# Kernel tuning notes

Measured on AMD Instinct MI355X. Metric: run time of the kernel, lower is better.

## Reference

```python
import jax, jax.numpy as jnp
import numpy as np

B, N, C, H = 8, 4096, 768, 8
EPS = 1e-12  # F.normalize eps


def setup_inputs() -> dict:
    key = jax.random.key(0)
    ks = jax.random.split(key, 4)
    x = jax.random.normal(ks[0], (B, N, C), dtype=jnp.float32)
    w_qkv = jax.random.normal(ks[1], (3 * C, C), dtype=jnp.float32) * 0.02
    temperature = jnp.ones((H, 1, 1), dtype=jnp.float32)
    w_proj = jax.random.normal(ks[2], (C, C), dtype=jnp.float32) * 0.02
    b_proj = jnp.zeros((C,), dtype=jnp.float32)
    return {"x": x, "w_qkv": w_qkv, "temperature": temperature,
            "w_proj": w_proj, "b_proj": b_proj}


def _l2norm(t):
    # F.normalize(t, dim=-1): t / max(||t||_2, eps)
    n = jnp.sqrt(jnp.sum(t * t, axis=-1, keepdims=True))
    return t / jnp.maximum(n, EPS)


def reference(x, w_qkv, temperature, w_proj, b_proj):
    b, n, c = x.shape
    h = H
    hd = c // h
    # qkv projection: (B,N,3C) -> (3,B,H,hd,N)
    qkv = (x @ w_qkv.T).reshape(b, n, 3, h, hd)
    qkv = jnp.transpose(qkv, (2, 0, 3, 4, 1))
    q, k, v = qkv[0], qkv[1], qkv[2]          # each (B,H,hd,N)
    qn = _l2norm(q)                            # normalize over N (token) dim
    kn = _l2norm(k)
    # small per-head covariance attention: (B,H,hd,hd)
    attn = jnp.einsum('bhdn,bhen->bhde', qn, kn) * temperature
    attn = jax.nn.softmax(attn, axis=-1)
    out = jnp.einsum('bhde,bhen->bhdn', attn, v)  # (B,H,hd,N)
    out = jnp.transpose(out, (0, 3, 1, 2)).reshape(b, n, c)
    return out @ w_proj.T + b_proj
```

## Files before the change

### kernel.cpp

```cpp
#include <hip/hip_runtime.h>
#include <cstdint>
#include <cstddef>

#define B_ 8
#define N_ 4096
#define C_ 768
#define H_ 8
#define HD_ 96
#define EPSN 1e-12f
#define NS_ 4

typedef short s16x8 __attribute__((ext_vector_type(8)));
typedef short s16x4 __attribute__((ext_vector_type(4)));
typedef float f32x4 __attribute__((ext_vector_type(4)));

static __device__ __forceinline__ short f2bf(float f) {
  unsigned u = __float_as_uint(f);
  unsigned r = (u + 0x7fff + ((u >> 16) & 1)) >> 16;
  return (short)r;
}
static __device__ __forceinline__ float bf2f(unsigned short s) {
  return __uint_as_float(((unsigned)s) << 16);
}
static __device__ __forceinline__ s16x8 pack8(const float4 a, const float4 b) {
  s16x8 r;
  r[0] = f2bf(a.x); r[1] = f2bf(a.y); r[2] = f2bf(a.z); r[3] = f2bf(a.w);
  r[4] = f2bf(b.x); r[5] = f2bf(b.y); r[6] = f2bf(b.z); r[7] = f2bf(b.w);
  return r;
}

#define TSW(ch, t) ((t) ^ ((((ch) >> 2) & 7) << 3))

static __device__ __forceinline__ int swz(int s) {
  return s ^ (((s >> 7) & 3) << 3);
}

static __device__ __forceinline__ void gld16(const short* g, short* l) {
  __builtin_amdgcn_global_load_lds(
      (const __attribute__((address_space(1))) void*)g,
      (__attribute__((address_space(3))) void*)l, 16, 0, 0);
}

__global__ __launch_bounds__(256)
void xcvt(const float* __restrict__ x, short* __restrict__ xb) {
  const int n8 = (B_ * N_ * C_) / 8;
  for (int i = blockIdx.x * 256 + threadIdx.x; i < n8; i += gridDim.x * 256) {
    const float4 a = *(const float4*)(x + (size_t)i * 8);
    const float4 b = *(const float4*)(x + (size_t)i * 8 + 4);
    *(s16x8*)(xb + (size_t)i * 8) = pack8(a, b);
  }
}

template<int BF>
__global__ __launch_bounds__(256)
void gram_p(const float* __restrict__ x, const short* __restrict__ xb,
            float* __restrict__ Gp) {
  const int f = blockIdx.x;
  const int xcd = f & 7;
  const int t = f >> 3;
  const int pair = t % 21;
  const int cdiv = t / 21;
  const int c = xcd + 8 * cdiv;
  const int split = c & 3;
  const int b = c >> 2;

  int rem = pair, ti = 0;
#pragma unroll
  for (int it = 0; it < 5; ++it)
    if (rem >= 6 - ti) { rem -= 6 - ti; ++ti; }
  const int tj = ti + rem;
  const int i0 = ti * 128, j0 = tj * 128;
  const bool diag = (ti == tj);

  const int tid = threadIdx.x;
  const int lane = tid & 63, wave = tid >> 6;
  const int l15 = lane & 15, quad = lane >> 4;
  const int wm = wave & 1, wn = wave >> 1;

  __shared__ __align__(16) short smem[2 * 128 * 72];
  short* At = smem;
  short* Bt = smem + 128 * 72;

  const int tg = tid >> 4;
  const int cg = tid & 15;
  const int t0 = tg * 4;
  const int c0 = cg * 4;
  const float* xbF = x + (size_t)b * N_ * C_;
  const short* xbB = xb + (size_t)b * N_ * C_;

  f32x4 acc[4][4] = {};

  const int nbeg = split * (N_ / NS_);
  const int nend = nbeg + (N_ / NS_);
  for (int n0 = nbeg; n0 < nend; n0 += 64) {
    if (BF) {
      s16x8 la[4], lb[4];
#pragma unroll
      for (int r = 0; r < 4; ++r)
        la[r] = *(const s16x8*)(xbB + (size_t)(n0 + t0 + r) * C_ + i0 + cg * 8);
      if (!diag) {
#pragma unroll
        for (int r = 0; r < 4; ++r)
          lb[r] = *(const s16x8*)(xbB + (size_t)(n0 + t0 + r) * C_ + j0 + cg * 8);
      }
      __syncthreads();
#pragma unroll
      for (int cc = 0; cc < 8; ++cc) {
        const int ch = cg * 8 + cc;
        s16x4 v;
        v[0] = la[0][cc]; v[1] = la[1][cc]; v[2] = la[2][cc]; v[3] = la[3][cc];
        *(s16x4*)&At[ch * 72 + TSW(ch, t0)] = v;
      }
      if (!diag) {
#pragma unroll
        for (int cc = 0; cc < 8; ++cc) {
          const int ch = cg * 8 + cc;
          s16x4 v;
          v[0] = lb[0][cc]; v[1] = lb[1][cc]; v[2] = lb[2][cc]; v[3] = lb[3][cc];
          *(s16x4*)&Bt[ch * 72 + TSW(ch, t0)] = v;
        }
      }
      __syncthreads();
    } else {
      float4 la[2][4], lb[2][4];
#pragma unroll
      for (int q = 0; q < 2; ++q)
#pragma unroll
        for (int r = 0; r < 4; ++r)
          la[q][r] = *(const float4*)(xbF + (size_t)(n0 + t0 + r) * C_ + i0 + c0 + q * 64);
      if (!diag) {
#pragma unroll
        for (int q = 0; q < 2; ++q)
#pragma unroll
          for (int r = 0; r < 4; ++r)
            lb[q][r] = *(const float4*)(xbF + (size_t)(n0 + t0 + r) * C_ + j0 + c0 + q * 64);
      }
      __syncthreads();
#pragma unroll
      for (int q = 0; q < 2; ++q)
#pragma unroll
        for (int cc = 0; cc < 4; ++cc) {
          const int ch = c0 + q * 64 + cc;
          s16x4 v;
          v[0] = f2bf(((const float*)&la[q][0])[cc]);
          v[1] = f2bf(((const float*)&la[q][1])[cc]);
          v[2] = f2bf(((const float*)&la[q][2])[cc]);
          v[3] = f2bf(((const float*)&la[q][3])[cc]);
          *(s16x4*)&At[ch * 72 + TSW(ch, t0)] = v;
        }
      if (!diag) {
#pragma unroll
        for (int q = 0; q < 2; ++q)
#pragma unroll
          for (int cc = 0; cc < 4; ++cc) {
            const int ch = c0 + q * 64 + cc;
            s16x4 v;
            v[0] = f2bf(((const float*)&lb[q][0])[cc]);
            v[1] = f2bf(((const float*)&lb[q][1])[cc]);
            v[2] = f2bf(((const float*)&lb[q][2])[cc]);
            v[3] = f2bf(((const float*)&lb[q][3])[cc]);
            *(s16x4*)&Bt[ch * 72 + TSW(ch, t0)] = v;
          }
      }
      __syncthreads();
    }
    const short* Bre = diag ? At : Bt;
#pragma unroll
    for (int ks = 0; ks < 64; ks += 32) {
      s16x8 af[4], bfr[4];
#pragma unroll
      for (int mi = 0; mi < 4; ++mi) {
        const int ch = wm * 64 + mi * 16 + l15;
        af[mi] = *(const s16x8*)&At[ch * 72 + TSW(ch, ks + quad * 8)];
      }
#pragma unroll
      for (int ni = 0; ni < 4; ++ni) {
        const int ch = wn * 64 + ni * 16 + l15;
        bfr[ni] = *(const s16x8*)&Bre[ch * 72 + TSW(ch, ks + quad * 8)];
      }
#pragma unroll
      for (int ni = 0; ni < 4; ++ni)
#pragma unroll
        for (int mi = 0; mi < 4; ++mi)
          acc[mi][ni] = __builtin_amdgcn_mfma_f32_16x16x32_bf16(af[mi], bfr[ni], acc[mi][ni], 0, 0, 0);
    }
    if (BF) __syncthreads();
  }

  float* Gpb = Gp + (((size_t)b * 21 + pair) * NS_ + split) * (128 * 128);
#pragma unroll
  for (int mi = 0; mi < 4; ++mi)
#pragma unroll
    for (int ni = 0; ni < 4; ++ni) {
      const int ii = wm * 64 + mi * 16 + quad * 4;
      const int jj = wn * 64 + ni * 16 + l15;
#pragma unroll
      for (int r = 0; r < 4; ++r)
        Gpb[(ii + r) * 128 + jj] = acc[mi][ni][r];
    }
}

__global__ __launch_bounds__(256)
void gram_red(const float* __restrict__ Gp, short* __restrict__ G) {
  const int pair = blockIdx.x;
  int rem = pair, ti = 0;
#pragma unroll
  for (int it = 0; it < 5; ++it)
    if (rem >= 6 - ti) { rem -= 6 - ti; ++ti; }
  const int tj = ti + rem;
  const int b = blockIdx.y;
  const int i0 = ti * 128, j0 = tj * 128;
  const bool diag = (ti == tj);
  const int tid = threadIdx.x;

  __shared__ short Ts[128 * 137];

  const float4* P = (const float4*)(Gp + (((size_t)b * 21 + pair) * NS_) * (128 * 128));
  short* Gb = G + (size_t)b * C_ * C_;

#pragma unroll
  for (int it = 0; it < 16; ++it) {
    const int q = tid + it * 256;
    const int row = q >> 5;
    const int c4 = q & 31;
    float4 v = P[q];
    const float4 v1 = P[q + 4096];
    const float4 v2 = P[q + 8192];
    const float4 v3 = P[q + 12288];
    v.x += v1.x + v2.x + v3.x;
    v.y += v1.y + v2.y + v3.y;
    v.z += v1.z + v2.z + v3.z;
    v.w += v1.w + v2.w + v3.w;
    s16x4 sv;
    sv[0] = f2bf(v.x); sv[1] = f2bf(v.y); sv[2] = f2bf(v.z); sv[3] = f2bf(v.w);
    *(s16x4*)&Gb[(size_t)(i0 + row) * C_ + j0 + c4 * 4] = sv;
    if (!diag) {
#pragma unroll
      for (int c = 0; c < 4; ++c)
        Ts[(c4 * 4 + c) * 137 + row] = sv[c];
    }
  }
  if (!diag) {
    __syncthreads();
#pragma unroll
    for (int p = 0; p < 8; ++p) {
      const int id = tid + p * 256;
      const int j = id >> 4, cs = (id & 15) * 8;
      *(s16x8*)&Gb[(size_t)(j0 + j) * C_ + i0 + cs] = *(const s16x8*)&Ts[j * 137 + cs];
    }
  }
}

__global__ __launch_bounds__(256)
void gemm_fb(const float* __restrict__ A, const short* __restrict__ Bb,
             short* __restrict__ Out, size_t sB, size_t sO) {
  const int z = blockIdx.z;
  const int n0 = blockIdx.x * 128;
  const int m0 = blockIdx.y * 128;
  const int tid = threadIdx.x;
  const int lane = tid & 63, wave = tid >> 6;
  const int l15 = lane & 15, quad = lane >> 4;
  const int wm = wave & 1, wn = wave >> 1;

  __shared__ __align__(16) short As[128 * 40];
  __shared__ __align__(16) short Bs[128 * 32];

  const int ar = tid >> 1;
  const int ak = (tid & 1) * 16;
  const float* ap = A + (size_t)(m0 + ar) * C_ + ak;

  const short* bsrc[2];
  short* bdst[2];
#pragma unroll
  for (int cc = 0; cc < 2; ++cc) {
    const int P = wave * 1024 + cc * 512 + lane * 8;
    const int L = swz(P);
    bsrc[cc] = Bb + (size_t)z * sB + (size_t)(n0 + (L >> 5)) * C_ + (L & 31);
    bdst[cc] = &Bs[wave * 1024 + cc * 512];
  }

  f32x4 acc[4][4] = {};

  for (int k0 = 0; k0 < C_; k0 += 32) {
    const float4 a0 = *(const float4*)(ap + k0 + 0);
    const float4 a1 = *(const float4*)(ap + k0 + 4);
    const float4 a2 = *(const float4*)(ap + k0 + 8);
    const float4 a3 = *(const float4*)(ap + k0 + 12);
    __syncthreads();
#pragma unroll
    for (int cc = 0; cc < 2; ++cc) gld16(bsrc[cc] + k0, bdst[cc]);
    *(s16x8*)&As[ar * 40 + ak]     = pack8(a0, a1);
    *(s16x8*)&As[ar * 40 + ak + 8] = pack8(a2, a3);
    __syncthreads();
    s16x8 af[4];
#pragma unroll
    for (int mi = 0; mi < 4; ++mi)
      af[mi] = *(const s16x8*)&As[(wm * 64 + mi * 16 + l15) * 40 + quad * 8];
#pragma unroll
    for (int ni = 0; ni < 4; ++ni) {
      const s16x8 bf = *(const s16x8*)&Bs[swz((wn * 64 + ni * 16 + l15) * 32 + quad * 8)];
#pragma unroll
      for (int mi = 0; mi < 4; ++mi)
        acc[mi][ni] = __builtin_amdgcn_mfma_f32_16x16x32_bf16(af[mi], bf, acc[mi][ni], 0, 0, 0);
    }
  }

  short* ob = Out + (size_t)z * sO;
#pragma unroll
  for (int mi = 0; mi < 4; ++mi) {
    const int m = m0 + wm * 64 + mi * 16 + quad * 4;
#pragma unroll
    for (int ni = 0; ni < 4; ++ni) {
      const int n = n0 + wn * 64 + ni * 16 + l15;
#pragma unroll
      for (int r = 0; r < 4; ++r)
        ob[(size_t)(m + r) * C_ + n] = f2bf(acc[mi][ni][r]);
    }
  }
}

__global__ __launch_bounds__(256)
void row_norms(const short* __restrict__ Y, const float* __restrict__ w_qkv,
               float* __restrict__ norms) {
  const int b = blockIdx.y;
  const int m = blockIdx.x * 4 + (threadIdx.x >> 6);
  const int lane = threadIdx.x & 63;
  const short* y = Y + ((size_t)b * 1536 + m) * C_;
  const float* w = w_qkv + (size_t)m * C_;
  float s = 0.f;
#pragma unroll
  for (int j = 0; j < 3; ++j) {
    const int o = j * 256 + lane * 4;
    const s16x4 yv = *(const s16x4*)(y + o);
    const float4 wv = *(const float4*)(w + o);
    s += bf2f((unsigned short)yv[0]) * wv.x + bf2f((unsigned short)yv[1]) * wv.y +
         bf2f((unsigned short)yv[2]) * wv.z + bf2f((unsigned short)yv[3]) * wv.w;
  }
#pragma unroll
  for (int o = 32; o > 0; o >>= 1) s += __shfl_xor(s, o);
  if (lane == 0) {
    int idx;
    if (m < 768) idx = (b * 8 + m / 96) * 96 + (m % 96);
    else { const int mm = m - 768; idx = B_ * H_ * 96 + (b * 8 + mm / 96) * 96 + (mm % 96); }
    norms[idx] = s;
  }
}

__global__ __launch_bounds__(256)
void s_attn(const short* __restrict__ Y, const float* __restrict__ w_qkv,
            const float* __restrict__ norms, const float* __restrict__ temp,
            float* __restrict__ S) {
  const int bh = blockIdx.x;
  const int b = bh >> 3, h = bh & 7;
  const int tid = threadIdx.x;
  const int lane = tid & 63, wave = tid >> 6;
  const int l15 = lane & 15, quad = lane >> 4;

  __shared__ __align__(16) float Sf[96 * 97];
  __shared__ float qsc[96], ksc[96];
  short* Ys = (short*)Sf;
  short* Ks = (short*)Sf + 96 * 72;

  if (tid < 96)
    qsc[tid] = temp[h] / fmaxf(sqrtf(norms[bh * 96 + tid]), EPSN);
  else if (tid < 192)
    ksc[tid - 96] = 1.0f / fmaxf(sqrtf(norms[B_ * H_ * 96 + bh * 96 + (tid - 96)]), EPSN);

  const short* yb = Y + ((size_t)b * 1536 + h * 96) * C_;
  const float* wk = w_qkv + (size_t)(C_ + h * 96) * C_;

  f32x4 sc[9] = {};
  for (int k0 = 0; k0 < C_; k0 += 64) {
    s16x8 yv[3];
    float4 wv[3][2];
#pragma unroll
    for (int j = 0; j < 3; ++j) {
      const int id = tid + j * 256;
      const int r = id >> 3, c8 = (id & 7) * 8;
      yv[j] = *(const s16x8*)(yb + (size_t)r * C_ + k0 + c8);
      wv[j][0] = *(const float4*)(wk + (size_t)r * C_ + k0 + c8);
      wv[j][1] = *(const float4*)(wk + (size_t)r * C_ + k0 + c8 + 4);
    }
    __syncthreads();
#pragma unroll
    for (int j = 0; j < 3; ++j) {
      const int id = tid + j * 256;
      const int r = id >> 3, c8 = (id & 7) * 8;
      *(s16x8*)&Ys[r * 72 + c8] = yv[j];
      *(s16x8*)&Ks[r * 72 + c8] = pack8(wv[j][0], wv[j][1]);
    }
    __syncthreads();
#pragma unroll
    for (int j = 0; j < 9; ++j) {
      const int t = wave * 9 + j, dt = t / 6, et = t % 6;
#pragma unroll
      for (int kk = 0; kk < 64; kk += 32) {
        const s16x8 a  = *(const s16x8*)&Ys[(dt * 16 + l15) * 72 + kk + quad * 8];
        const s16x8 bb = *(const s16x8*)&Ks[(et * 16 + l15) * 72 + kk + quad * 8];
        sc[j] = __builtin_amdgcn_mfma_f32_16x16x32_bf16(a, bb, sc[j], 0, 0, 0);
      }
    }
  }
  __syncthreads();
#pragma unroll
  for (int j = 0; j < 9; ++j) {
    const int t = wave * 9 + j, dt = t / 6, et = t % 6;
    const int e = et * 16 + l15;
    const float kf = ksc[e];
#pragma unroll
    for (int r = 0; r < 4; ++r) {
      const int d = dt * 16 + quad * 4 + r;
      Sf[d * 97 + e] = sc[j][r] * qsc[d] * kf;
    }
  }
  __syncthreads();
  float* Sb = S + (size_t)bh * (HD_ * HD_);
  for (int rr = 0; rr < 24; ++rr) {
    const int d = wave * 24 + rr;
    const float v0 = Sf[d * 97 + lane];
    const float v1 = (lane < 32) ? Sf[d * 97 + 64 + lane] : -1e30f;
    float mx = fmaxf(v0, v1);
#pragma unroll
    for (int o = 32; o > 0; o >>= 1) mx = fmaxf(mx, __shfl_xor(mx, o));
    const float e0 = __expf(v0 - mx);
    const float e1 = (lane < 32) ? __expf(v1 - mx) : 0.0f;
    float sum = e0 + e1;
#pragma unroll
    for (int o = 32; o > 0; o >>= 1) sum += __shfl_xor(sum, o);
    const float inv = 1.0f / sum;
    Sb[d * 96 + lane] = e0 * inv;
    if (lane < 32) Sb[d * 96 + 64 + lane] = e1 * inv;
  }
}

__global__ __launch_bounds__(256)
void av_gemm(const float* __restrict__ S, const float* __restrict__ w_qkv,
             short* __restrict__ AVt) {
  const int bh = blockIdx.x;
  const int b = bh >> 3, h = bh & 7;
  const int ct = blockIdx.y * 64;
  const int tid = threadIdx.x;
  __shared__ float at[96 * 97];
  __shared__ float wv[96 * 64];
  const float* Sb = S + (size_t)bh * (HD_ * HD_);
  for (int i = tid; i < 96 * 96; i += 256)
    at[(i / 96) * 97 + (i % 96)] = Sb[i];
  for (int i = tid; i < 96 * 64; i += 256) {
    const int e = i >> 6, c = i & 63;
    wv[e * 64 + c] = w_qkv[(size_t)(2 * C_ + h * 96 + e) * C_ + ct + c];
  }
  __syncthreads();
  const int d0 = (tid >> 4) * 6;
  const int c0 = (tid & 15) * 4;
  float acc[6][4] = {};
  for (int e = 0; e < 96; ++e) {
    const float4 bv = *(const float4*)&wv[e * 64 + c0];
    float aa[6];
#pragma unroll
    for (int i = 0; i < 6; ++i) aa[i] = at[(d0 + i) * 97 + e];
#pragma unroll
    for (int i = 0; i < 6; ++i) {
      acc[i][0] += aa[i] * bv.x; acc[i][1] += aa[i] * bv.y;
      acc[i][2] += aa[i] * bv.z; acc[i][3] += aa[i] * bv.w;
    }
  }
  short* AVb = AVt + (size_t)b * C_ * C_;
#pragma unroll
  for (int i = 0; i < 6; ++i)
#pragma unroll
    for (int j = 0; j < 4; ++j)
      AVb[(size_t)(ct + c0 + j) * C_ + h * 96 + d0 + i] = f2bf(acc[i][j]);
}

__global__ __launch_bounds__(256)
void gemm_xm_bf(const short* __restrict__ xb, const short* __restrict__ Mb,
                const float* __restrict__ bias, float* __restrict__ out) {
  const int f = blockIdx.x;
  const int xcd = f & 7;
  const int t = f >> 3;
  const int j6 = t % 6;
  const int sdiv = t / 6;
  const int s = xcd + 8 * sdiv;
  const int z = s >> 5;
  const int n0 = j6 * 128;
  const int m0 = (s & 31) * 128;
  const int tid = threadIdx.x;
  const int lane = tid & 63;
  const int wave = tid >> 6;
  const int l15 = lane & 15;
  const int quad = lane >> 4;
  const int wm = wave & 1;
  const int wn = wave >> 1;

  __shared__ __align__(16) short As[128 * 32];
  __shared__ __align__(16) short Bs[128 * 32];

  const short* asrc[2]; const short* bsrc[2];
  short* adst[2]; short* bdst[2];
#pragma unroll
  for (int cc = 0; cc < 2; ++cc) {
    const int P = wave * 1024 + cc * 512 + lane * 8;
    const int L = swz(P);
    const int row = L >> 5, col = L & 31;
    asrc[cc] = xb + ((size_t)z * N_ + m0 + row) * C_ + col;
    bsrc[cc] = Mb + (size_t)z * C_ * C_ + (size_t)(n0 + row) * C_ + col;
    adst[cc] = &As[wave * 1024 + cc * 512];
    bdst[cc] = &Bs[wave * 1024 + cc * 512];
  }

  f32x4 acc[4][4] = {};

  for (int k0 = 0; k0 < C_; k0 += 32) {
    __syncthreads();
#pragma unroll
    for (int cc = 0; cc < 2; ++cc) {
      gld16(asrc[cc] + k0, adst[cc]);
      gld16(bsrc[cc] + k0, bdst[cc]);
    }
    __syncthreads();
    s16x8 af[4];
#pragma unroll
    for (int mi = 0; mi < 4; ++mi)
      af[mi] = *(const s16x8*)&As[swz((wm * 64 + mi * 16 + l15) * 32 + quad * 8)];
#pragma unroll
    for (int ni = 0; ni < 4; ++ni) {
      const s16x8 bf = *(const s16x8*)&Bs[swz((wn * 64 + ni * 16 + l15) * 32 + quad * 8)];
#pragma unroll
      for (int mi = 0; mi < 4; ++mi)
        acc[mi][ni] = __builtin_amdgcn_mfma_f32_16x16x32_bf16(af[mi], bf, acc[mi][ni], 0, 0, 0);
    }
  }

  float bv[4];
#pragma unroll
  for (int ni = 0; ni < 4; ++ni) bv[ni] = bias[n0 + wn * 64 + ni * 16 + l15];
#pragma unroll
  for (int mi = 0; mi < 4; ++mi) {
    const int m = m0 + wm * 64 + mi * 16 + quad * 4;
#pragma unroll
    for (int ni = 0; ni < 4; ++ni) {
      const int n = n0 + wn * 64 + ni * 16 + l15;
      float* dst = out + ((size_t)z * N_ + m) * C_ + n;
#pragma unroll
      for (int r = 0; r < 4; ++r)
        dst[(size_t)r * C_] = acc[mi][ni][r] + bv[ni];
    }
  }
}

__global__ __launch_bounds__(256)
void gemm_xm_f32(const float* __restrict__ x, const short* __restrict__ Mb,
                 const float* __restrict__ bias, float* __restrict__ out) {
  const int f = blockIdx.x;
  const int xcd = f & 7;
  const int t = f >> 3;
  const int j6 = t % 6;
  const int sdiv = t / 6;
  const int s = xcd + 8 * sdiv;
  const int z = s >> 5;
  const int n0 = j6 * 128;
  const int m0 = (s & 31) * 128;
  const int tid = threadIdx.x;
  const int lane = tid & 63;
  const int wave = tid >> 6;
  const int l15 = lane & 15;
  const int quad = lane >> 4;
  const int wm = wave & 1;
  const int wn = wave >> 1;

  __shared__ __align__(16) short As[128 * 40];
  __shared__ __align__(16) short Bs[128 * 40];

  const int ar = tid >> 1;
  const int ak = (tid & 1) * 16;
  const float* xp = x + ((size_t)z * N_ + m0 + ar) * C_ + ak;
  const short* mp = Mb + (size_t)z * C_ * C_ + (size_t)(n0 + ar) * C_ + ak;

  f32x4 acc[4][4] = {};

  for (int k0 = 0; k0 < C_; k0 += 32) {
    const float4 a0 = *(const float4*)(xp + k0 + 0);
    const float4 a1 = *(const float4*)(xp + k0 + 4);
    const float4 a2 = *(const float4*)(xp + k0 + 8);
    const float4 a3 = *(const float4*)(xp + k0 + 12);
    const s16x8 b0 = *(const s16x8*)(mp + k0 + 0);
    const s16x8 b1 = *(const s16x8*)(mp + k0 + 8);
    __syncthreads();
    *(s16x8*)&As[ar * 40 + ak]     = pack8(a0, a1);
    *(s16x8*)&As[ar * 40 + ak + 8] = pack8(a2, a3);
    *(s16x8*)&Bs[ar * 40 + ak]     = b0;
    *(s16x8*)&Bs[ar * 40 + ak + 8] = b1;
    __syncthreads();
    s16x8 af[4];
#pragma unroll
    for (int mi = 0; mi < 4; ++mi)
      af[mi] = *(const s16x8*)&As[(wm * 64 + mi * 16 + l15) * 40 + quad * 8];
#pragma unroll
    for (int ni = 0; ni < 4; ++ni) {
      const s16x8 bf = *(const s16x8*)&Bs[(wn * 64 + ni * 16 + l15) * 40 + quad * 8];
#pragma unroll
      for (int mi = 0; mi < 4; ++mi)
        acc[mi][ni] = __builtin_amdgcn_mfma_f32_16x16x32_bf16(af[mi], bf, acc[mi][ni], 0, 0, 0);
    }
  }

  float bv[4];
#pragma unroll
  for (int ni = 0; ni < 4; ++ni) bv[ni] = bias[n0 + wn * 64 + ni * 16 + l15];
#pragma unroll
  for (int mi = 0; mi < 4; ++mi) {
    const int m = m0 + wm * 64 + mi * 16 + quad * 4;
#pragma unroll
    for (int ni = 0; ni < 4; ++ni) {
      const int n = n0 + wn * 64 + ni * 16 + l15;
      float* dst = out + ((size_t)z * N_ + m) * C_ + n;
#pragma unroll
      for (int r = 0; r < 4; ++r)
        dst[(size_t)r * C_] = acc[mi][ni][r] + bv[ni];
    }
  }
}

extern "C" void kernel_launch(void* const* d_in, const int* in_sizes, int n_in,
                              void* d_out, int out_size, void* d_ws, size_t ws_size,
                              hipStream_t stream) {
  const float* x      = (const float*)d_in[0];
  const float* w_qkv  = (const float*)d_in[1];
  const float* temp   = (const float*)d_in[2];
  const float* w_proj = (const float*)d_in[3];
  const float* b_proj = (const float*)d_in[4];
  float* out = (float*)d_out;

  char* base = (char*)d_ws;
  float* S     = (float*)base;
  float* norms = (float*)(base + 2359296);
  short* G     = (short*)(base + 2408448);
  short* AVt   = G;
  short* Mb    = (short*)(base + 11845632);
  short* Y     = (short*)(base + 21282816);

  const size_t need1 = 55885824 + 50331648;
  const size_t need2 = 40157184 + 50331648;
  const int tier = (ws_size >= need1) ? 1 : (ws_size >= need2) ? 2 : 3;

  float* Gp = (tier == 2) ? (float*)(base + 40157184) : (float*)(base + 11845632);
  short* xb = (tier == 1) ? (short*)(base + 55885824)
            : (tier == 2) ? (short*)(base + 40157184) : nullptr;

  if (tier == 1) {
    xcvt<<<3072, 256, 0, stream>>>(x, xb);
    gram_p<1><<<21 * NS_ * B_, 256, 0, stream>>>(x, xb, Gp);
  } else {
    gram_p<0><<<21 * NS_ * B_, 256, 0, stream>>>(x, xb ? xb : (const short*)G, Gp);
  }

  gram_red<<<dim3(21, B_), 256, 0, stream>>>(Gp, G);

  if (tier == 2) xcvt<<<3072, 256, 0, stream>>>(x, xb);

  gemm_fb<<<dim3(C_ / 128, 1536 / 128, B_), 256, 0, stream>>>(
      w_qkv, G, Y, (size_t)C_ * C_, (size_t)1536 * C_);

  row_norms<<<dim3(1536 / 4, B_), 256, 0, stream>>>(Y, w_qkv, norms);

  s_attn<<<B_ * H_, 256, 0, stream>>>(Y, w_qkv, norms, temp, S);

  av_gemm<<<dim3(B_ * H_, C_ / 64), 256, 0, stream>>>(S, w_qkv, AVt);

  gemm_fb<<<dim3(C_ / 128, C_ / 128, B_), 256, 0, stream>>>(
      w_proj, AVt, Mb, (size_t)C_ * C_, (size_t)C_ * C_);

  if (tier == 3)
    gemm_xm_f32<<<C_ / 128 * (N_ / 128) * B_, 256, 0, stream>>>(x, Mb, b_proj, out);
  else
    gemm_xm_bf<<<C_ / 128 * (N_ / 128) * B_, 256, 0, stream>>>(xb, Mb, b_proj, out);
}
```

Measured before the change: 430.6 us.

## Double-buffer GEMM LDS tiles, pre-convert w_qkv to bf16, widen s_attn

```diff
diff --git a/kernel.cpp b/kernel.cpp
--- a/kernel.cpp
+++ b/kernel.cpp
@@ -49,6 +49,14 @@
     const float4 b = *(const float4*)(x + (size_t)i * 8 + 4);
     *(s16x8*)(xb + (size_t)i * 8) = pack8(a, b);
   }
+}
+
+__global__ __launch_bounds__(256)
+void wcvt(const float* __restrict__ w, short* __restrict__ wb) {
+  const int i = blockIdx.x * 256 + threadIdx.x;
+  const float4 a = *(const float4*)(w + (size_t)i * 8);
+  const float4 b = *(const float4*)(w + (size_t)i * 8 + 4);
+  *(s16x8*)(wb + (size_t)i * 8) = pack8(a, b);
 }
 
 template<int BF>
@@ -184,7 +192,6 @@
         for (int mi = 0; mi < 4; ++mi)
           acc[mi][ni] = __builtin_amdgcn_mfma_f32_16x16x32_bf16(af[mi], bfr[ni], acc[mi][ni], 0, 0, 0);
     }
-    if (BF) __syncthreads();
   }
 
   float* Gpb = Gp + (((size_t)b * 21 + pair) * NS_ + split) * (128 * 128);
@@ -252,6 +259,79 @@
 }
 
 __global__ __launch_bounds__(256)
+void gemm_nt_bf(const short* __restrict__ A, const short* __restrict__ Bb,
+                short* __restrict__ Out, size_t sB, size_t sO) {
+  const int z = blockIdx.z;
+  const int n0 = blockIdx.x * 128;
+  const int m0 = blockIdx.y * 128;
+  const int tid = threadIdx.x;
+  const int lane = tid & 63, wave = tid >> 6;
+  const int l15 = lane & 15, quad = lane >> 4;
+  const int wm = wave & 1, wn = wave >> 1;
+
+  __shared__ __align__(16) short As[2][128 * 32];
+  __shared__ __align__(16) short Bs[2][128 * 32];
+
+  const short* asrc[2]; const short* bsrc[2];
+  int doff[2];
+#pragma unroll
+  for (int cc = 0; cc < 2; ++cc) {
+    const int P = wave * 1024 + cc * 512 + lane * 8;
+    const int L = swz(P);
+    const int row = L >> 5, col = L & 31;
+    asrc[cc] = A + (size_t)(m0 + row) * C_ + col;
+    bsrc[cc] = Bb + (size_t)z * sB + (size_t)(n0 + row) * C_ + col;
+    doff[cc] = wave * 1024 + cc * 512;
+  }
+
+  f32x4 acc[4][4] = {};
+
+#pragma unroll
+  for (int cc = 0; cc < 2; ++cc) {
+    gld16(asrc[cc], &As[0][doff[cc]]);
+    gld16(bsrc[cc], &Bs[0][doff[cc]]);
+  }
+  __syncthreads();
+  int cur = 0;
+  for (int k0 = 0; k0 < C_; k0 += 32) {
+    const int nx = k0 + 32;
+    if (nx < C_) {
+#pragma unroll
+      for (int cc = 0; cc < 2; ++cc) {
+        gld16(asrc[cc] + nx, &As[cur ^ 1][doff[cc]]);
+        gld16(bsrc[cc] + nx, &Bs[cur ^ 1][doff[cc]]);
+      }
+    }
+    s16x8 af[4];
+#pragma unroll
+    for (int mi = 0; mi < 4; ++mi)
+      af[mi] = *(const s16x8*)&As[cur][swz((wm * 64 + mi * 16 + l15) * 32 + quad * 8)];
+#pragma unroll
+    for (int ni = 0; ni < 4; ++ni) {
+      const s16x8 bf = *(const s16x8*)&Bs[cur][swz((wn * 64 + ni * 16 + l15) * 32 + quad * 8)];
+#pragma unroll
+      for (int mi = 0; mi < 4; ++mi)
+        acc[mi][ni] = __builtin_amdgcn_mfma_f32_16x16x32_bf16(af[mi], bf, acc[mi][ni], 0, 0, 0);
+    }
+    __syncthreads();
+    cur ^= 1;
+  }
+
+  short* ob = Out + (size_t)z * sO;
+#pragma unroll
+  for (int mi = 0; mi < 4; ++mi) {
+    const int m = m0 + wm * 64 + mi * 16 + quad * 4;
+#pragma unroll
+    for (int ni = 0; ni < 4; ++ni) {
+      const int n = n0 + wn * 64 + ni * 16 + l15;
+#pragma unroll
+      for (int r = 0; r < 4; ++r)
+        ob[(size_t)(m + r) * C_ + n] = f2bf(acc[mi][ni][r]);
+    }
+  }
+}
+
+__global__ __launch_bounds__(256)
 void gemm_fb(const float* __restrict__ A, const short* __restrict__ Bb,
              short* __restrict__ Out, size_t sB, size_t sO) {
   const int z = blockIdx.z;
@@ -262,47 +342,65 @@
   const int l15 = lane & 15, quad = lane >> 4;
   const int wm = wave & 1, wn = wave >> 1;
 
-  __shared__ __align__(16) short As[128 * 40];
-  __shared__ __align__(16) short Bs[128 * 32];
+  __shared__ __align__(16) short As[2][128 * 40];
+  __shared__ __align__(16) short Bs[2][128 * 32];
 
   const int ar = tid >> 1;
   const int ak = (tid & 1) * 16;
   const float* ap = A + (size_t)(m0 + ar) * C_ + ak;
 
   const short* bsrc[2];
-  short* bdst[2];
+  int doff[2];
 #pragma unroll
   for (int cc = 0; cc < 2; ++cc) {
     const int P = wave * 1024 + cc * 512 + lane * 8;
     const int L = swz(P);
     bsrc[cc] = Bb + (size_t)z * sB + (size_t)(n0 + (L >> 5)) * C_ + (L & 31);
-    bdst[cc] = &Bs[wave * 1024 + cc * 512];
+    doff[cc] = wave * 1024 + cc * 512;
   }
 
   f32x4 acc[4][4] = {};
 
+  {
+    const float4 a0 = *(const float4*)(ap + 0);
+    const float4 a1 = *(const float4*)(ap + 4);
+    const float4 a2 = *(const float4*)(ap + 8);
+    const float4 a3 = *(const float4*)(ap + 12);
+#pragma unroll
+    for (int cc = 0; cc < 2; ++cc) gld16(bsrc[cc], &Bs[0][doff[cc]]);
+    *(s16x8*)&As[0][ar * 40 + ak]     = pack8(a0, a1);
+    *(s16x8*)&As[0][ar * 40 + ak + 8] = pack8(a2, a3);
+  }
+  __syncthreads();
+  int cur = 0;
   for (int k0 = 0; k0 < C_; k0 += 32) {
-    const float4 a0 = *(const float4*)(ap + k0 + 0);
-    const float4 a1 = *(const float4*)(ap + k0 + 4);
-    const float4 a2 = *(const float4*)(ap + k0 + 8);
-    const float4 a3 = *(const float4*)(ap + k0 + 12);
-    __syncthreads();
-#pragma unroll
-    for (int cc = 0; cc < 2; ++cc) gld16(bsrc[cc] + k0, bdst[cc]);
-    *(s16x8*)&As[ar * 40 + ak]     = pack8(a0, a1);
-    *(s16x8*)&As[ar * 40 + ak + 8] = pack8(a2, a3);
-    __syncthreads();
+    const int nx = k0 + 32;
+    float4 a0, a1, a2, a3;
+    if (nx < C_) {
+      a0 = *(const float4*)(ap + nx + 0);
+      a1 = *(const float4*)(ap + nx + 4);
+      a2 = *(const float4*)(ap + nx + 8);
+      a3 = *(const float4*)(ap + nx + 12);
+#pragma unroll
+      for (int cc = 0; cc < 2; ++cc) gld16(bsrc[cc] + nx, &Bs[cur ^ 1][doff[cc]]);
+    }
     s16x8 af[4];
 #pragma unroll
     for (int mi = 0; mi < 4; ++mi)
-      af[mi] = *(const s16x8*)&As[(wm * 64 + mi * 16 + l15) * 40 + quad * 8];
-#pragma unroll
-    for (int ni = 0; ni < 4; ++ni) {
-      const s16x8 bf = *(const s16x8*)&Bs[swz((wn * 64 + ni * 16 + l15) * 32 + quad * 8)];
+      af[mi] = *(const s16x8*)&As[cur][(wm * 64 + mi * 16 + l15) * 40 + quad * 8];
+#pragma unroll
+    for (int ni = 0; ni < 4; ++ni) {
+      const s16x8 bf = *(const s16x8*)&Bs[cur][swz((wn * 64 + ni * 16 + l15) * 32 + quad * 8)];
 #pragma unroll
       for (int mi = 0; mi < 4; ++mi)
         acc[mi][ni] = __builtin_amdgcn_mfma_f32_16x16x32_bf16(af[mi], bf, acc[mi][ni], 0, 0, 0);
     }
+    if (nx < C_) {
+      *(s16x8*)&As[cur ^ 1][ar * 40 + ak]     = pack8(a0, a1);
+      *(s16x8*)&As[cur ^ 1][ar * 40 + ak + 8] = pack8(a2, a3);
+    }
+    __syncthreads();
+    cur ^= 1;
   }
 
   short* ob = Out + (size_t)z * sO;
@@ -346,8 +444,8 @@
   }
 }
 
-__global__ __launch_bounds__(256)
-void s_attn(const short* __restrict__ Y, const float* __restrict__ w_qkv,
+__global__ __launch_bounds__(512)
+void s_attn(const short* __restrict__ Y, const short* __restrict__ wb,
             const float* __restrict__ norms, const float* __restrict__ temp,
             float* __restrict__ S) {
   const int bh = blockIdx.x;
@@ -367,56 +465,66 @@
     ksc[tid - 96] = 1.0f / fmaxf(sqrtf(norms[B_ * H_ * 96 + bh * 96 + (tid - 96)]), EPSN);
 
   const short* yb = Y + ((size_t)b * 1536 + h * 96) * C_;
-  const float* wk = w_qkv + (size_t)(C_ + h * 96) * C_;
-
-  f32x4 sc[9] = {};
+  const short* kb = wb + (size_t)(768 + h * 96) * C_;
+
+  int dts[5], ets[5];
+#pragma unroll
+  for (int j = 0; j < 5; ++j) {
+    const int t = j * 8 + wave;
+    dts[j] = t / 6; ets[j] = t % 6;
+  }
+
+  f32x4 sc[5] = {};
+  const int r0 = tid >> 3, c80 = (tid & 7) * 8;
+  const int id1 = tid + 512;
+  const int r1 = id1 >> 3, c81 = (id1 & 7) * 8;
   for (int k0 = 0; k0 < C_; k0 += 64) {
-    s16x8 yv[3];
-    float4 wv[3][2];
-#pragma unroll
-    for (int j = 0; j < 3; ++j) {
-      const int id = tid + j * 256;
-      const int r = id >> 3, c8 = (id & 7) * 8;
-      yv[j] = *(const s16x8*)(yb + (size_t)r * C_ + k0 + c8);
-      wv[j][0] = *(const float4*)(wk + (size_t)r * C_ + k0 + c8);
-      wv[j][1] = *(const float4*)(wk + (size_t)r * C_ + k0 + c8 + 4);
+    s16x8 yv0, kv0, yv1, kv1;
+    yv0 = *(const s16x8*)(yb + (size_t)r0 * C_ + k0 + c80);
+    kv0 = *(const s16x8*)(kb + (size_t)r0 * C_ + k0 + c80);
+    if (tid < 256) {
+      yv1 = *(const s16x8*)(yb + (size_t)r1 * C_ + k0 + c81);
+      kv1 = *(const s16x8*)(kb + (size_t)r1 * C_ + k0 + c81);
     }
     __syncthreads();
-#pragma unroll
-    for (int j = 0; j < 3; ++j) {
-      const int id = tid + j * 256;
-      const int r = id >> 3, c8 = (id & 7) * 8;
-      *(s16x8*)&Ys[r * 72 + c8] = yv[j];
-      *(s16x8*)&Ks[r * 72 + c8] = pack8(wv[j][0], wv[j][1]);
+    *(s16x8*)&Ys[r0 * 72 + c80] = yv0;
+    *(s16x8*)&Ks[r0 * 72 + c80] = kv0;
+    if (tid < 256) {
+      *(s16x8*)&Ys[r1 * 72 + c81] = yv1;
+      *(s16x8*)&Ks[r1 * 72 + c81] = kv1;
     }
     __syncthreads();
 #pragma unroll
-    for (int j = 0; j < 9; ++j) {
-      const int t = wave * 9 + j, dt = t / 6, et = t % 6;
-#pragma unroll
-      for (int kk = 0; kk < 64; kk += 32) {
-        const s16x8 a  = *(const s16x8*)&Ys[(dt * 16 + l15) * 72 + kk + quad * 8];
-        const s16x8 bb = *(const s16x8*)&Ks[(et * 16 + l15) * 72 + kk + quad * 8];
-        sc[j] = __builtin_amdgcn_mfma_f32_16x16x32_bf16(a, bb, sc[j], 0, 0, 0);
+    for (int j = 0; j < 5; ++j) {
+      const int t = j * 8 + wave;
+      if (t < 36) {
+#pragma unroll
+        for (int kk = 0; kk < 64; kk += 32) {
+          const s16x8 a  = *(const s16x8*)&Ys[(dts[j] * 16 + l15) * 72 + kk + quad * 8];
+          const s16x8 bb = *(const s16x8*)&Ks[(ets[j] * 16 + l15) * 72 + kk + quad * 8];
+          sc[j] = __builtin_amdgcn_mfma_f32_16x16x32_bf16(a, bb, sc[j], 0, 0, 0);
+        }
       }
     }
   }
   __syncthreads();
 #pragma unroll
-  for (int j = 0; j < 9; ++j) {
-    const int t = wave * 9 + j, dt = t / 6, et = t % 6;
-    const int e = et * 16 + l15;
-    const float kf = ksc[e];
-#pragma unroll
-    for (int r = 0; r < 4; ++r) {
-      const int d = dt * 16 + quad * 4 + r;
-      Sf[d * 97 + e] = sc[j][r] * qsc[d] * kf;
+  for (int j = 0; j < 5; ++j) {
+    const int t = j * 8 + wave;
+    if (t < 36) {
+      const int e = ets[j] * 16 + l15;
+      const float kf = ksc[e];
+#pragma unroll
+      for (int r = 0; r < 4; ++r) {
+        const int d = dts[j] * 16 + quad * 4 + r;
+        Sf[d * 97 + e] = sc[j][r] * qsc[d] * kf;
+      }
     }
   }
   __syncthreads();
   float* Sb = S + (size_t)bh * (HD_ * HD_);
-  for (int rr = 0; rr < 24; ++rr) {
-    const int d = wave * 24 + rr;
+  for (int rr = 0; rr < 12; ++rr) {
+    const int d = wave * 12 + rr;
     const float v0 = Sf[d * 97 + lane];
     const float v1 = (lane < 32) ? Sf[d * 97 + 64 + lane] : -1e30f;
     float mx = fmaxf(v0, v1);
@@ -492,11 +600,11 @@
   const int wm = wave & 1;
   const int wn = wave >> 1;
 
-  __shared__ __align__(16) short As[128 * 32];
-  __shared__ __align__(16) short Bs[128 * 32];
+  __shared__ __align__(16) short As[2][128 * 32];
+  __shared__ __align__(16) short Bs[2][128 * 32];
 
   const short* asrc[2]; const short* bsrc[2];
-  short* adst[2]; short* bdst[2];
+  int doff[2];
 #pragma unroll
   for (int cc = 0; cc < 2; ++cc) {
     const int P = wave * 1024 + cc * 512 + lane * 8;
@@ -504,31 +612,40 @@
     const int row = L >> 5, col = L & 31;
     asrc[cc] = xb + ((size_t)z * N_ + m0 + row) * C_ + col;
     bsrc[cc] = Mb + (size_t)z * C_ * C_ + (size_t)(n0 + row) * C_ + col;
-    adst[cc] = &As[wave * 1024 + cc * 512];
-    bdst[cc] = &Bs[wave * 1024 + cc * 512];
+    doff[cc] = wave * 1024 + cc * 512;
   }
 
   f32x4 acc[4][4] = {};
 
+#pragma unroll
+  for (int cc = 0; cc < 2; ++cc) {
+    gld16(asrc[cc], &As[0][doff[cc]]);
+    gld16(bsrc[cc], &Bs[0][doff[cc]]);
+  }
+  __syncthreads();
+  int cur = 0;
   for (int k0 = 0; k0 < C_; k0 += 32) {
-    __syncthreads();
-#pragma unroll
-    for (int cc = 0; cc < 2; ++cc) {
-      gld16(asrc[cc] + k0, adst[cc]);
-      gld16(bsrc[cc] + k0, bdst[cc]);
-    }
-    __syncthreads();
+    const int nx = k0 + 32;
+    if (nx < C_) {
+#pragma unroll
+      for (int cc = 0; cc < 2; ++cc) {
+        gld16(asrc[cc] + nx, &As[cur ^ 1][doff[cc]]);
+        gld16(bsrc[cc] + nx, &Bs[cur ^ 1][doff[cc]]);
+      }
+    }
     s16x8 af[4];
 #pragma unroll
     for (int mi = 0; mi < 4; ++mi)
-      af[mi] = *(const s16x8*)&As[swz((wm * 64 + mi * 16 + l15) * 32 + quad * 8)];
-#pragma unroll
-    for (int ni = 0; ni < 4; ++ni) {
-      const s16x8 bf = *(const s16x8*)&Bs[swz((wn * 64 + ni * 16 + l15) * 32 + quad * 8)];
+      af[mi] = *(const s16x8*)&As[cur][swz((wm * 64 + mi * 16 + l15) * 32 + quad * 8)];
+#pragma unroll
+    for (int ni = 0; ni < 4; ++ni) {
+      const s16x8 bf = *(const s16x8*)&Bs[cur][swz((wn * 64 + ni * 16 + l15) * 32 + quad * 8)];
 #pragma unroll
       for (int mi = 0; mi < 4; ++mi)
         acc[mi][ni] = __builtin_amdgcn_mfma_f32_16x16x32_bf16(af[mi], bf, acc[mi][ni], 0, 0, 0);
     }
+    __syncthreads();
+    cur ^= 1;
   }
 
   float bv[4];
@@ -638,6 +755,7 @@
   short* AVt   = G;
   short* Mb    = (short*)(base + 11845632);
   short* Y     = (short*)(base + 21282816);
+  short* wb    = (short*)(base + 11845632);
 
   const size_t need1 = 55885824 + 50331648;
   const size_t need2 = 40157184 + 50331648;
@@ -658,12 +776,14 @@
 
   if (tier == 2) xcvt<<<3072, 256, 0, stream>>>(x, xb);
 
-  gemm_fb<<<dim3(C_ / 128, 1536 / 128, B_), 256, 0, stream>>>(
-      w_qkv, G, Y, (size_t)C_ * C_, (size_t)1536 * C_);
+  wcvt<<<576, 256, 0, stream>>>(w_qkv, wb);
+
+  gemm_nt_bf<<<dim3(C_ / 128, 1536 / 128, B_), 256, 0, stream>>>(
+      wb, G, Y, (size_t)C_ * C_, (size_t)1536 * C_);
 
   row_norms<<<dim3(1536 / 4, B_), 256, 0, stream>>>(Y, w_qkv, norms);
 
-  s_attn<<<B_ * H_, 256, 0, stream>>>(Y, w_qkv, norms, temp, S);
+  s_attn<<<B_ * H_, 512, 0, stream>>>(Y, wb, norms, temp, S);
 
   av_gemm<<<dim3(B_ * H_, C_ / 64), 256, 0, stream>>>(S, w_qkv, AVt);
 
```

Result: faster. 399.1 us (-7.3%).
